# Kernel optimization log

Hardware: AMD Instinct MI355X
Metric: run time of the kernel (lower is better)

Reference implementation:

```python
import jax, jax.numpy as jnp
import numpy as np

GROUP_SIZE = 64
SCALING = 32.0 / 16.0  # lora_alpha / r


def setup_inputs() -> dict:
    key = jax.random.key(0)
    k = jax.random.split(key, 7)
    B, S, I, O, R = 4, 2048, 4096, 4096, 16
    G = I // GROUP_SIZE
    x = jax.random.normal(k[0], (B, S, I), dtype=jnp.float32)
    W_q = jax.random.randint(k[1], (O, I), 0, 16, dtype=jnp.int32)
    scale = jax.random.uniform(k[2], (O, G), dtype=jnp.float32) * 0.01 + 1e-4
    zero = jax.random.uniform(k[3], (O, G), dtype=jnp.float32) * 8.0
    lora_A = jax.random.normal(k[4], (I, R), dtype=jnp.float32) * 0.02
    lora_B = jax.random.normal(k[5], (R, O), dtype=jnp.float32) * 0.02
    bias = jax.random.normal(k[6], (O,), dtype=jnp.float32) * 0.01
    return {"x": x, "W_q": W_q, "scale": scale, "zero": zero,
            "lora_A": lora_A, "lora_B": lora_B, "bias": bias}


def reference(x, W_q, scale, zero, lora_A, lora_B, bias):
    O, I = W_q.shape
    G = I // GROUP_SIZE
    # HQQ-style group-wise affine dequant: W = (W_q - zero) * scale  -> [O, I]
    Wg = W_q.reshape(O, G, GROUP_SIZE).astype(scale.dtype)
    W = ((Wg - zero[:, :, None]) * scale[:, :, None]).reshape(O, I)
    # base quantized linear: out = x @ W^T
    out = jnp.einsum('bsi,oi->bso', x, W)
    # LoRA low-rank update (dropout is Identity for p=0)
    out = out + (x @ lora_A @ lora_B) * SCALING
    # bias add
    out = out + bias
    return out
```

## Files before the change

kernel.cpp:

```cpp
#include <hip/hip_runtime.h>
#include <hip/hip_bf16.h>
#include <stdint.h>

#define M_DIM 8192
#define N_DIM 4096
#define K_DIM 4096

typedef __attribute__((ext_vector_type(8))) __bf16 bf16x8;
typedef __attribute__((ext_vector_type(4))) float f32x4;

__device__ inline unsigned short f2bf(float f) {
  unsigned u = __builtin_bit_cast(unsigned, f);
  u += 0x7FFF + ((u >> 16) & 1);
  return (unsigned short)(u >> 16);
}

__device__ inline void async_copy16(const void* g, void* l) {
  __builtin_amdgcn_global_load_lds(
      (const __attribute__((address_space(1))) unsigned int*)g,
      (__attribute__((address_space(3))) unsigned int*)l, 16, 0, 0);
}

__global__ __launch_bounds__(256) void prep_kernel(
    const float* __restrict__ x, unsigned short* __restrict__ xb,
    const int* __restrict__ Wq, const float* __restrict__ scale,
    const float* __restrict__ zero, const float* __restrict__ A,
    const float* __restrict__ Bm, unsigned short* __restrict__ Weff) {
  int t = threadIdx.x;
  if (blockIdx.x < 4096) {
    __shared__ float sA[64 * 17];
    __shared__ float sB[16 * 64];
    int bo = blockIdx.x >> 6;
    int bi = blockIdx.x & 63;
    int o0 = bo * 64, i0 = bi * 64;
    for (int j = t; j < 1024; j += 256) sA[(j >> 4) * 17 + (j & 15)] = A[i0 * 16 + j];
    for (int j = t; j < 1024; j += 256) sB[j] = Bm[(j >> 6) * N_DIM + o0 + (j & 63)];
    __syncthreads();
    for (int e = 0; e < 16; ++e) {
      int idx = e * 256 + t;
      int oo = idx >> 6, ii = idx & 63;
      int o = o0 + oo;
      float sc = scale[o * 64 + bi];
      float zp = zero[o * 64 + bi];
      float w = ((float)Wq[(size_t)o * K_DIM + i0 + ii] - zp) * sc;
      float acc = 0.f;
#pragma unroll
      for (int r = 0; r < 16; ++r) acc += sA[ii * 17 + r] * sB[r * 64 + oo];
      w += 2.0f * acc;
      Weff[(size_t)o * K_DIM + i0 + ii] = f2bf(w);
    }
  } else {
    int i = (blockIdx.x - 4096) * 256 + t;
    int stride = 2048 * 256;
    int n4 = (M_DIM * K_DIM) / 4;
    for (; i < n4; i += stride) {
      float4 v = reinterpret_cast<const float4*>(x)[i];
      ushort4 o;
      o.x = f2bf(v.x); o.y = f2bf(v.y); o.z = f2bf(v.z); o.w = f2bf(v.w);
      reinterpret_cast<ushort4*>(xb)[i] = o;
    }
  }
}

#define BAR() __builtin_amdgcn_s_barrier()
#define SB()  __builtin_amdgcn_sched_barrier(0)
#define WAIT_VM4() do { asm volatile("s_waitcnt vmcnt(4)" ::: "memory"); } while (0)

__device__ __forceinline__ bf16x8 lds_frag(const unsigned short* region, int row, int c) {
  return *reinterpret_cast<const bf16x8*>(region + row * 64 + ((c ^ (row & 7)) << 3));
}

__device__ __forceinline__ void readA(const unsigned short* reg, int mh, int lc, int lr,
                                      bf16x8 a[4][2]) {
#pragma unroll
  for (int m = 0; m < 4; ++m) {
    int row = mh * 64 + m * 16 + lc;
#pragma unroll
    for (int kk = 0; kk < 2; ++kk) a[m][kk] = lds_frag(reg, row, kk * 4 + lr);
  }
}

__device__ __forceinline__ void readB(const unsigned short* reg, int nh, int rB, int lc, int lr,
                                      bf16x8 b[2][2]) {
#pragma unroll
  for (int n = 0; n < 2; ++n) {
    int row = rB + (nh * 2 + n) * 16 + lc;
#pragma unroll
    for (int kk = 0; kk < 2; ++kk) b[n][kk] = lds_frag(reg, row, kk * 4 + lr);
  }
}

__device__ __forceinline__ void mfma_quad(const bf16x8 a[4][2], const bf16x8 b[2][2],
                                          f32x4 acc[8][4], int mh, int nh) {
  __builtin_amdgcn_s_setprio(1);
#pragma unroll
  for (int kk = 0; kk < 2; ++kk)
#pragma unroll
    for (int m = 0; m < 4; ++m)
#pragma unroll
      for (int n = 0; n < 2; ++n)
        acc[mh * 4 + m][nh * 2 + n] = __builtin_amdgcn_mfma_f32_16x16x32_bf16(
            a[m][kk], b[n][kk], acc[mh * 4 + m][nh * 2 + n], 0, 0, 0);
  __builtin_amdgcn_s_setprio(0);
}

__global__ __launch_bounds__(512, 2) void gemm_kernel(
    const unsigned short* __restrict__ xb, const unsigned short* __restrict__ wb,
    const float* __restrict__ bias, float* __restrict__ out) {
  __shared__ unsigned short lds[65536];

  int bid = blockIdx.x;
  int swz = (bid & 7) * 64 + (bid >> 3);
  int mt = swz >> 4, nt = swz & 15;
  int m0 = mt * 256, n0 = nt * 256;

  int tid = threadIdx.x;
  int w = tid >> 6, lane = tid & 63;
  int wr = w >> 2, wc = w & 3;
  int lr = lane >> 4, lc = lane & 15;
  int rB = (wc & 1) * 64;

  int r0 = tid >> 3, c0g = (tid & 7) ^ (r0 & 7);
  int co0 = tid * 8, co1 = (512 + tid) * 8;

  const unsigned short* sA00 = xb + (size_t)(m0 + r0) * K_DIM + c0g * 8;
  const unsigned short* sB00 = wb + (size_t)(n0 + r0) * K_DIM + c0g * 8;

#define STAGE_A(h, buf, kt) do { \
    const unsigned short* _p = sA00 + (size_t)(h) * 128 * K_DIM + (size_t)(kt); \
    async_copy16(_p, &lds[(buf) * 32768 + (h) * 8192 + co0]); \
    async_copy16(_p + (size_t)64 * K_DIM, &lds[(buf) * 32768 + (h) * 8192 + co1]); } while (0)
#define STAGE_B(h, buf, kt) do { \
    const unsigned short* _p = sB00 + (size_t)(h) * 128 * K_DIM + (size_t)(kt); \
    async_copy16(_p, &lds[(buf) * 32768 + 16384 + (h) * 8192 + co0]); \
    async_copy16(_p + (size_t)64 * K_DIM, &lds[(buf) * 32768 + 16384 + (h) * 8192 + co1]); } while (0)

  const unsigned short* aR[2] = { &lds[wr * 8192], &lds[32768 + wr * 8192] };
  const unsigned short* bR[2] = { &lds[16384 + (wc >> 1) * 8192],
                                  &lds[32768 + 16384 + (wc >> 1) * 8192] };

  f32x4 acc[8][4];
#pragma unroll
  for (int i = 0; i < 8; ++i)
#pragma unroll
    for (int j = 0; j < 4; ++j) acc[i][j] = f32x4{0.f, 0.f, 0.f, 0.f};

  STAGE_B(0, 0, 0); STAGE_B(1, 0, 0); STAGE_A(0, 0, 0); STAGE_A(1, 0, 0);
  STAGE_B(0, 1, 64); STAGE_B(1, 1, 64); STAGE_A(0, 1, 64);
  asm volatile("s_waitcnt vmcnt(6)" ::: "memory");
  BAR(); SB();
  bf16x8 aU[4][2], aV[4][2], b0[2][2], b1[2][2];
  readA(aR[0], 0, lc, lr, aU); readB(bR[0], 0, rB, lc, lr, b0);
  SB();

#pragma unroll 1
  for (int i = 0; i < 32; ++i) {
    int k1 = (2 * i + 1) * 64;
    int k2 = ((2 * i + 2) & 63) * 64;
    int k3 = ((2 * i + 3) & 63) * 64;

    readB(bR[0], 1, rB, lc, lr, b1);
    SB(); STAGE_A(1, 1, k1); SB();
    mfma_quad(aU, b0, acc, 0, 0);
    SB(); BAR(); SB();
    readA(aR[0], 1, lc, lr, aV);
    SB(); STAGE_B(0, 0, k2); SB();
    mfma_quad(aU, b1, acc, 0, 1);
    SB(); BAR(); SB();
    SB(); STAGE_B(1, 0, k2); SB();
    mfma_quad(aV, b0, acc, 1, 0);
    SB(); WAIT_VM4(); BAR(); SB();
    readA(aR[1], 0, lc, lr, aU); readB(bR[1], 0, rB, lc, lr, b0);
    SB(); STAGE_A(0, 0, k2); SB();
    mfma_quad(aV, b1, acc, 1, 1);
    SB(); BAR(); SB();
    readB(bR[1], 1, rB, lc, lr, b1);
    SB(); STAGE_A(1, 0, k2); SB();
    mfma_quad(aU, b0, acc, 0, 0);
    SB(); BAR(); SB();
    readA(aR[1], 1, lc, lr, aV);
    SB(); STAGE_B(0, 1, k3); SB();
    mfma_quad(aU, b1, acc, 0, 1);
    SB(); BAR(); SB();
    SB(); STAGE_B(1, 1, k3); SB();
    mfma_quad(aV, b0, acc, 1, 0);
    SB(); WAIT_VM4(); BAR(); SB();
    readA(aR[0], 0, lc, lr, aU); readB(bR[0], 0, rB, lc, lr, b0);
    SB(); STAGE_A(0, 1, k3); SB();
    mfma_quad(aV, b1, acc, 1, 1);
    SB(); BAR(); SB();
  }
  asm volatile("s_waitcnt vmcnt(0) lgkmcnt(0)" ::: "memory");

#pragma unroll
  for (int ni = 0; ni < 4; ++ni) {
    int n = n0 + wc * 64 + ni * 16 + lc;
    float bv = bias[n];
#pragma unroll
    for (int mi = 0; mi < 8; ++mi) {
      int mb = m0 + wr * 128 + mi * 16 + lr * 4;
#pragma unroll
      for (int j = 0; j < 4; ++j)
        out[(size_t)(mb + j) * N_DIM + n] = acc[mi][ni][j] + bv;
    }
  }
#undef STAGE_A
#undef STAGE_B
}

extern "C" void kernel_launch(void* const* d_in, const int* in_sizes, int n_in,
                              void* d_out, int out_size, void* d_ws, size_t ws_size,
                              hipStream_t stream) {
  const float* x     = (const float*)d_in[0];
  const int*   Wq    = (const int*)d_in[1];
  const float* scale = (const float*)d_in[2];
  const float* zero  = (const float*)d_in[3];
  const float* lA    = (const float*)d_in[4];
  const float* lB    = (const float*)d_in[5];
  const float* bias  = (const float*)d_in[6];
  float* out = (float*)d_out;

  unsigned short* xb = (unsigned short*)d_ws;
  unsigned short* wb = (unsigned short*)((char*)d_ws + (size_t)M_DIM * K_DIM * 2);

  prep_kernel<<<6144, 256, 0, stream>>>(x, xb, Wq, scale, zero, lA, lB, wb);
  gemm_kernel<<<512, 512, 0, stream>>>(xb, wb, bias, out);
}
```

Before: 310.5 us.

## Vectorize weight prep, relax GEMM sched barriers, drop setprio, nontemporal stores

The weight dequant+LoRA prep now has each thread handle 8 contiguous elements, using 128-bit int4 loads and paired ushort4 stores instead of scalar loads and stores, with the sB value reused across them. In the GEMM main loop, many sched_barrier fences around the async copies are removed, so the compiler can interleave global-to-LDS copies with MFMAs. The s_setprio bumps around the MFMA blocks are dropped. Output stores become nontemporal. Looser scheduling fences could let the compiler reorder LDS reads or copies against barriers in unexpected ways.

```diff
diff --git a/kernel.cpp b/kernel.cpp
--- a/kernel.cpp
+++ b/kernel.cpp
@@ -36,18 +36,30 @@
     for (int j = t; j < 1024; j += 256) sA[(j >> 4) * 17 + (j & 15)] = A[i0 * 16 + j];
     for (int j = t; j < 1024; j += 256) sB[j] = Bm[(j >> 6) * N_DIM + o0 + (j & 63)];
     __syncthreads();
-    for (int e = 0; e < 16; ++e) {
-      int idx = e * 256 + t;
-      int oo = idx >> 6, ii = idx & 63;
+#pragma unroll
+    for (int e = 0; e < 2; ++e) {
+      int slot = e * 256 + t;
+      int oo = slot >> 3, ii0 = (slot & 7) * 8;
       int o = o0 + oo;
       float sc = scale[o * 64 + bi];
       float zp = zero[o * 64 + bi];
-      float w = ((float)Wq[(size_t)o * K_DIM + i0 + ii] - zp) * sc;
-      float acc = 0.f;
-#pragma unroll
-      for (int r = 0; r < 16; ++r) acc += sA[ii * 17 + r] * sB[r * 64 + oo];
-      w += 2.0f * acc;
-      Weff[(size_t)o * K_DIM + i0 + ii] = f2bf(w);
+      const int* qp = &Wq[(size_t)o * K_DIM + i0 + ii0];
+      int4 q0 = *reinterpret_cast<const int4*>(qp);
+      int4 q1 = *reinterpret_cast<const int4*>(qp + 4);
+      int qv[8] = {q0.x, q0.y, q0.z, q0.w, q1.x, q1.y, q1.z, q1.w};
+      ushort4 r0, r1;
+      unsigned short rr[8];
+#pragma unroll
+      for (int j = 0; j < 8; ++j) {
+        float acc = 0.f;
+#pragma unroll
+        for (int r = 0; r < 16; ++r) acc += sA[(ii0 + j) * 17 + r] * sB[r * 64 + oo];
+        rr[j] = f2bf(((float)qv[j] - zp) * sc + 2.0f * acc);
+      }
+      r0 = ushort4{rr[0], rr[1], rr[2], rr[3]};
+      r1 = ushort4{rr[4], rr[5], rr[6], rr[7]};
+      ushort4* wp = reinterpret_cast<ushort4*>(&Weff[(size_t)o * K_DIM + i0 + ii0]);
+      wp[0] = r0; wp[1] = r1;
     }
   } else {
     int i = (blockIdx.x - 4096) * 256 + t;
@@ -92,7 +104,6 @@
 
 __device__ __forceinline__ void mfma_quad(const bf16x8 a[4][2], const bf16x8 b[2][2],
                                           f32x4 acc[8][4], int mh, int nh) {
-  __builtin_amdgcn_s_setprio(1);
 #pragma unroll
   for (int kk = 0; kk < 2; ++kk)
 #pragma unroll
@@ -101,7 +112,6 @@
       for (int n = 0; n < 2; ++n)
         acc[mh * 4 + m][nh * 2 + n] = __builtin_amdgcn_mfma_f32_16x16x32_bf16(
             a[m][kk], b[n][kk], acc[mh * 4 + m][nh * 2 + n], 0, 0, 0);
-  __builtin_amdgcn_s_setprio(0);
 }
 
 __global__ __launch_bounds__(512, 2) void gemm_kernel(
@@ -148,10 +158,9 @@
   STAGE_B(0, 0, 0); STAGE_B(1, 0, 0); STAGE_A(0, 0, 0); STAGE_A(1, 0, 0);
   STAGE_B(0, 1, 64); STAGE_B(1, 1, 64); STAGE_A(0, 1, 64);
   asm volatile("s_waitcnt vmcnt(6)" ::: "memory");
-  BAR(); SB();
+  SB(); BAR(); SB();
   bf16x8 aU[4][2], aV[4][2], b0[2][2], b1[2][2];
   readA(aR[0], 0, lc, lr, aU); readB(bR[0], 0, rB, lc, lr, b0);
-  SB();
 
 #pragma unroll 1
   for (int i = 0; i < 32; ++i) {
@@ -160,35 +169,35 @@
     int k3 = ((2 * i + 3) & 63) * 64;
 
     readB(bR[0], 1, rB, lc, lr, b1);
-    SB(); STAGE_A(1, 1, k1); SB();
+    STAGE_A(1, 1, k1);
     mfma_quad(aU, b0, acc, 0, 0);
-    SB(); BAR(); SB();
+    BAR(); SB();
     readA(aR[0], 1, lc, lr, aV);
-    SB(); STAGE_B(0, 0, k2); SB();
+    STAGE_B(0, 0, k2);
     mfma_quad(aU, b1, acc, 0, 1);
-    SB(); BAR(); SB();
-    SB(); STAGE_B(1, 0, k2); SB();
+    BAR(); SB();
+    STAGE_B(1, 0, k2);
     mfma_quad(aV, b0, acc, 1, 0);
-    SB(); WAIT_VM4(); BAR(); SB();
+    WAIT_VM4(); SB(); BAR(); SB();
     readA(aR[1], 0, lc, lr, aU); readB(bR[1], 0, rB, lc, lr, b0);
-    SB(); STAGE_A(0, 0, k2); SB();
+    STAGE_A(0, 0, k2);
     mfma_quad(aV, b1, acc, 1, 1);
-    SB(); BAR(); SB();
+    BAR(); SB();
     readB(bR[1], 1, rB, lc, lr, b1);
-    SB(); STAGE_A(1, 0, k2); SB();
+    STAGE_A(1, 0, k2);
     mfma_quad(aU, b0, acc, 0, 0);
-    SB(); BAR(); SB();
+    BAR(); SB();
     readA(aR[1], 1, lc, lr, aV);
-    SB(); STAGE_B(0, 1, k3); SB();
+    STAGE_B(0, 1, k3);
     mfma_quad(aU, b1, acc, 0, 1);
-    SB(); BAR(); SB();
-    SB(); STAGE_B(1, 1, k3); SB();
+    BAR(); SB();
+    STAGE_B(1, 1, k3);
     mfma_quad(aV, b0, acc, 1, 0);
-    SB(); WAIT_VM4(); BAR(); SB();
+    WAIT_VM4(); SB(); BAR(); SB();
     readA(aR[0], 0, lc, lr, aU); readB(bR[0], 0, rB, lc, lr, b0);
-    SB(); STAGE_A(0, 1, k3); SB();
+    STAGE_A(0, 1, k3);
     mfma_quad(aV, b1, acc, 1, 1);
-    SB(); BAR(); SB();
+    BAR(); SB();
   }
   asm volatile("s_waitcnt vmcnt(0) lgkmcnt(0)" ::: "memory");
 
@@ -201,7 +210,8 @@
       int mb = m0 + wr * 128 + mi * 16 + lr * 4;
 #pragma unroll
       for (int j = 0; j < 4; ++j)
-        out[(size_t)(mb + j) * N_DIM + n] = acc[mi][ni][j] + bv;
+        __builtin_nontemporal_store(acc[mi][ni][j] + bv,
+                                    &out[(size_t)(mb + j) * N_DIM + n]);
     }
   }
 #undef STAGE_A
```

Measured after the change: 282.9 us. -8.9%, faster.
